# Optimization experiments

Hardware: AMD Instinct MI355X
Metric: run time of the kernel (lower is better)

The kernel has to match this reference:

```python
import jax, jax.numpy as jnp
import numpy as np

BS, C, T, H, W = 1, 64, 4, 24, 24
CH = C // 2  # half channels = 32


def setup_inputs() -> dict:
    key = jax.random.key(0)
    ks = jax.random.split(key, 6)
    s = 0.05  # small init scale keeps softmax logits well-conditioned
    return {
        "x": jax.random.normal(ks[0], (BS, C, T, H, W), dtype=jnp.float32),
        "theta_w": jax.random.normal(ks[1], (CH, C), dtype=jnp.float32) * s,
        "theta_b": jnp.zeros((CH,), dtype=jnp.float32),
        "phi_w": jax.random.normal(ks[2], (CH, C), dtype=jnp.float32) * s,
        "phi_b": jnp.zeros((CH,), dtype=jnp.float32),
        "g_w": jax.random.normal(ks[3], (CH, C), dtype=jnp.float32) * s,
        "g_b": jnp.zeros((CH,), dtype=jnp.float32),
        "k_w": jax.random.normal(ks[4], (C, CH), dtype=jnp.float32) * s,
        "k_b": jnp.zeros((C,), dtype=jnp.float32),
    }


def reference(x, theta_w, theta_b, phi_w, phi_b, g_w, g_b, k_w, k_b):
    bs, c_in, t, h, w = x.shape
    n = t * h * w
    xr = x.reshape(bs, c_in, n)  # 1x1x1 conv3d == per-position channel matmul
    v1 = jnp.einsum('oc,bcn->bon', theta_w, xr) + theta_b[:, None]  # (bs, C/2, N)
    v2 = jnp.einsum('oc,bcn->bon', phi_w, xr) + phi_b[:, None]      # (bs, C/2, N)
    gv = jnp.einsum('oc,bcn->bon', g_w, xr) + g_b[:, None]          # (bs, C/2, N)
    # per-channel rank-1 scores: score[b,c,i,j] = v1[b,c,i] * v2[b,c,j]
    scores = v1[:, :, :, None] * v2[:, :, None, :]                   # (bs, C/2, N, N)
    weights = jax.nn.softmax(scores, axis=-1)
    y = jnp.einsum('bcnm,bcm->bcn', weights, gv)                     # (bs, C/2, N)
    z = jnp.einsum('oc,bcn->bon', k_w, y) + k_b[:, None]             # (bs, C, N)
    return x + z.reshape(bs, c_in, t, h, w)
```

## Files before the change

### kernel.cpp

```cpp
#include <hip/hip_runtime.h>

#define N      2304
#define CIN    64
#define CHALF  32
#define KT     17
#define TILE   32
#define NBLK   (N / TILE)
#define NCOEF  (2 * KT * CHALF)
#define WPAD   36

__device__ __constant__ float INVF_C[KT] = {
    1.0f, 1.0f, 0.5f, 1.6666667e-1f, 4.1666668e-2f, 8.3333333e-3f,
    1.3888889e-3f, 1.9841270e-4f, 2.4801587e-5f, 2.7557319e-6f,
    2.7557319e-7f, 2.5052108e-8f, 2.0876756e-9f, 1.6059044e-10f,
    1.1470746e-11f, 7.6471637e-13f, 4.7794773e-14f };

__global__ __launch_bounds__(256) void k_momA(
    const float* __restrict__ x,
    const float* __restrict__ pw, const float* __restrict__ pb,
    const float* __restrict__ gw, const float* __restrict__ gb,
    float* __restrict__ partial)
{
    __shared__ float xs[CIN][TILE];
    __shared__ float wt2[2][CIN][WPAD];
    __shared__ float bs2[2][CHALF];
    __shared__ float bl[CHALF][33];
    __shared__ float gl[CHALF][33];

    const int tid = threadIdx.x;
    const int blk = blockIdx.x;
    const int n0  = blk * TILE;

    for (int idx = tid; idx < CIN * TILE; idx += 256) {
        int c = idx >> 5, nn = idx & 31;
        xs[c][nn] = x[c * N + n0 + nn];
    }
    for (int idx = tid; idx < 2 * CHALF * CIN; idx += 256) {
        int p = idx >> 11, rem = idx & 2047;
        int co = rem >> 6, c = rem & 63;
        wt2[p][c][co] = (p ? gw : pw)[rem];
    }
    if (tid < 2 * CHALF) {
        int p = tid >> 5, co = tid & 31;
        bs2[p][co] = (p ? gb : pb)[co];
    }
    __syncthreads();

    {
        const int pos = tid & 31;
        const int g8  = tid >> 5;
        float ab[4] = {0.f,0.f,0.f,0.f}, ag[4] = {0.f,0.f,0.f,0.f};
        #pragma unroll 4
        for (int c = 0; c < CIN; ++c) {
            float  xv = xs[c][pos];
            float4 wb = *(const float4*)&wt2[0][c][g8 * 4];
            float4 wg = *(const float4*)&wt2[1][c][g8 * 4];
            ab[0] = fmaf(wb.x, xv, ab[0]); ab[1] = fmaf(wb.y, xv, ab[1]);
            ab[2] = fmaf(wb.z, xv, ab[2]); ab[3] = fmaf(wb.w, xv, ab[3]);
            ag[0] = fmaf(wg.x, xv, ag[0]); ag[1] = fmaf(wg.y, xv, ag[1]);
            ag[2] = fmaf(wg.z, xv, ag[2]); ag[3] = fmaf(wg.w, xv, ag[3]);
        }
        #pragma unroll
        for (int k = 0; k < 4; ++k) {
            int co = g8 * 4 + k;
            bl[co][pos] = ab[k] + bs2[0][co];
            gl[co][pos] = ag[k] + bs2[1][co];
        }
    }
    __syncthreads();

    {
        const int c  = tid & 31;
        const int kg = tid >> 5;
        const int k1 = kg + 1, k2 = kg + 9;
        float d1 = 0.f, n1 = 0.f, d2 = 0.f, n2 = 0.f, n0s = 0.f;
        #pragma unroll 8
        for (int pos = 0; pos < TILE; ++pos) {
            float b  = bl[c][pos];
            float g  = gl[c][pos];
            float b2 = b * b, b4 = b2 * b2, b8 = b4 * b4;
            float p1 = (k1 & 1) ? b : 1.0f;
            p1 = (k1 & 2) ? p1 * b2 : p1;
            p1 = (k1 & 4) ? p1 * b4 : p1;
            p1 = (k1 & 8) ? p1 * b8 : p1;
            float p2 = p1 * b8;
            d1 += p1; n1 = fmaf(p1, g, n1);
            d2 += p2; n2 = fmaf(p2, g, n2);
            n0s += g;
        }
        float* pp = partial + blk * NCOEF;
        pp[k1 * 32 + c]       = d1;
        pp[544 + k1 * 32 + c] = n1;
        pp[k2 * 32 + c]       = d2;
        pp[544 + k2 * 32 + c] = n2;
        if (kg == 0) {
            pp[c]       = (float)TILE;
            pp[544 + c] = n0s;
        }
    }
}

__global__ __launch_bounds__(256) void k_evalB(
    const float* __restrict__ x,
    const float* __restrict__ tw, const float* __restrict__ tb,
    const float* __restrict__ kw, const float* __restrict__ kb,
    const float* __restrict__ partial,
    float* __restrict__ out)
{
    __shared__ float xs[CIN][TILE];
    __shared__ float wtt[CIN][WPAD];
    __shared__ float kws[CIN * CHALF];
    __shared__ float tbs[CHALF];
    __shared__ float cfl[NCOEF];
    __shared__ float al[CHALF][40];
    __shared__ float ys[CHALF][33];

    const int tid = threadIdx.x;
    const int n0  = blockIdx.x * TILE;

    for (int idx = tid; idx < CIN * TILE; idx += 256) {
        int c = idx >> 5, nn = idx & 31;
        xs[c][nn] = x[c * N + n0 + nn];
    }
    for (int idx = tid; idx < CHALF * CIN; idx += 256) {
        int co = idx >> 6, c = idx & 63;
        wtt[c][co] = tw[idx];
    }
    for (int idx = tid; idx < CIN * CHALF; idx += 256)
        kws[idx] = kw[idx];
    if (tid < CHALF) tbs[tid] = tb[tid];

    for (int t = tid; t < NCOEF / 4; t += 256) {
        float4 v = make_float4(0.f, 0.f, 0.f, 0.f);
        for (int s = 0; s < NBLK; ++s) {
            float4 p = *(const float4*)&partial[s * NCOEF + t * 4];
            v.x += p.x; v.y += p.y; v.z += p.z; v.w += p.w;
        }
        int idx = t * 4;
        int k = (idx < 544) ? (idx >> 5) : ((idx - 544) >> 5);
        float f = INVF_C[k];
        v.x *= f; v.y *= f; v.z *= f; v.w *= f;
        *(float4*)&cfl[idx] = v;
    }
    __syncthreads();

    {
        const int pos = tid & 31;
        const int g8  = tid >> 5;
        float aa[4] = {0.f,0.f,0.f,0.f};
        #pragma unroll 4
        for (int c = 0; c < CIN; ++c) {
            float  xv = xs[c][pos];
            float4 wv = *(const float4*)&wtt[c][g8 * 4];
            aa[0] = fmaf(wv.x, xv, aa[0]); aa[1] = fmaf(wv.y, xv, aa[1]);
            aa[2] = fmaf(wv.z, xv, aa[2]); aa[3] = fmaf(wv.w, xv, aa[3]);
        }
        #pragma unroll
        for (int k = 0; k < 4; ++k) {
            int co = g8 * 4 + k;
            al[co][pos] = aa[k] + tbs[co];
        }
    }
    __syncthreads();

    {
        const int c = tid >> 3;
        const int l = tid & 7;
        float dc[KT], nc[KT];
        #pragma unroll
        for (int k = 0; k < KT; ++k) {
            dc[k] = cfl[k * 32 + c];
            nc[k] = cfl[544 + k * 32 + c];
        }
        #pragma unroll
        for (int p = 0; p < 4; ++p) {
            int   ii = l + 8 * p;
            float a  = al[c][ii];
            float den = dc[KT - 1], num = nc[KT - 1];
            #pragma unroll
            for (int k = KT - 2; k >= 0; --k) {
                den = fmaf(den, a, dc[k]);
                num = fmaf(num, a, nc[k]);
            }
            ys[c][ii] = num / den;
        }
    }
    __syncthreads();

    {
        const int ii = tid & 31;
        const int cg = tid >> 5;
        float yv[CHALF];
        #pragma unroll
        for (int c = 0; c < CHALF; ++c) yv[c] = ys[c][ii];

        #pragma unroll
        for (int p = 0; p < 8; ++p) {
            int   co = cg * 8 + p;
            float z  = kb[co];
            const float4* kr = (const float4*)&kws[co * CHALF];
            #pragma unroll
            for (int c4 = 0; c4 < CHALF / 4; ++c4) {
                float4 kv = kr[c4];
                z = fmaf(kv.x, yv[c4 * 4 + 0], z);
                z = fmaf(kv.y, yv[c4 * 4 + 1], z);
                z = fmaf(kv.z, yv[c4 * 4 + 2], z);
                z = fmaf(kv.w, yv[c4 * 4 + 3], z);
            }
            out[co * N + n0 + ii] = xs[co][ii] + z;
        }
    }
}

extern "C" void kernel_launch(void* const* d_in, const int* in_sizes, int n_in,
                              void* d_out, int out_size, void* d_ws, size_t ws_size,
                              hipStream_t stream)
{
    const float* x  = (const float*)d_in[0];
    const float* tw = (const float*)d_in[1];
    const float* tb = (const float*)d_in[2];
    const float* pw = (const float*)d_in[3];
    const float* pb = (const float*)d_in[4];
    const float* gw = (const float*)d_in[5];
    const float* gb = (const float*)d_in[6];
    const float* kw = (const float*)d_in[7];
    const float* kb = (const float*)d_in[8];
    float* out = (float*)d_out;

    float* partial = (float*)d_ws;

    k_momA<<<dim3(NBLK), dim3(256), 0, stream>>>(
        x, pw, pb, gw, gb, partial);

    k_evalB<<<dim3(NBLK), dim3(256), 0, stream>>>(
        x, tw, tb, kw, kb, partial, out);
}
```

Baseline: 24.18 us.

## Move theta projection into first kernel and register-tile channel matmuls

The theta projection (v1) is now computed in the moment kernel alongside phi and g and written to workspace, so the evaluation kernel no longer loads x and theta weights to recompute it. Both 1x1 channel matmuls now use 4x4 register tiles with float4 shared-memory loads in place of per-position scalar loops. The output projection splits the channel reduction across two thread halves and combines them through shared memory. This trades extra global traffic for v1 and an added barrier against less redundant staging and more arithmetic per shared-memory load.

Result: faster. 22.84 us (-5.6%).

```diff
diff --git a/kernel.cpp b/kernel.cpp
--- a/kernel.cpp
+++ b/kernel.cpp
@@ -7,7 +7,7 @@
 #define TILE   32
 #define NBLK   (N / TILE)
 #define NCOEF  (2 * KT * CHALF)
-#define WPAD   36
+#define NCOL   (NCOEF / 4)
 
 __device__ __constant__ float INVF_C[KT] = {
     1.0f, 1.0f, 0.5f, 1.6666667e-1f, 4.1666668e-2f, 8.3333333e-3f,
@@ -17,15 +17,16 @@
 
 __global__ __launch_bounds__(256) void k_momA(
     const float* __restrict__ x,
+    const float* __restrict__ tw, const float* __restrict__ tb,
     const float* __restrict__ pw, const float* __restrict__ pb,
     const float* __restrict__ gw, const float* __restrict__ gb,
-    float* __restrict__ partial)
+    float* __restrict__ v1, float* __restrict__ partial)
 {
     __shared__ float xs[CIN][TILE];
-    __shared__ float wt2[2][CIN][WPAD];
-    __shared__ float bs2[2][CHALF];
-    __shared__ float bl[CHALF][33];
-    __shared__ float gl[CHALF][33];
+    __shared__ float wt3[3][CIN][36];
+    __shared__ float bs3[3][CHALF];
+    __shared__ float bl[CHALF][36];
+    __shared__ float gl[CHALF][36];
 
     const int tid = threadIdx.x;
     const int blk = blockIdx.x;
@@ -35,36 +36,56 @@
         int c = idx >> 5, nn = idx & 31;
         xs[c][nn] = x[c * N + n0 + nn];
     }
-    for (int idx = tid; idx < 2 * CHALF * CIN; idx += 256) {
+    for (int idx = tid; idx < 3 * CHALF * CIN; idx += 256) {
         int p = idx >> 11, rem = idx & 2047;
         int co = rem >> 6, c = rem & 63;
-        wt2[p][c][co] = (p ? gw : pw)[rem];
-    }
-    if (tid < 2 * CHALF) {
+        const float* w = (p == 0) ? tw : (p == 1) ? pw : gw;
+        wt3[p][c][co] = w[rem];
+    }
+    if (tid < 3 * CHALF) {
         int p = tid >> 5, co = tid & 31;
-        bs2[p][co] = (p ? gb : pb)[co];
-    }
-    __syncthreads();
-
-    {
-        const int pos = tid & 31;
-        const int g8  = tid >> 5;
-        float ab[4] = {0.f,0.f,0.f,0.f}, ag[4] = {0.f,0.f,0.f,0.f};
+        const float* b = (p == 0) ? tb : (p == 1) ? pb : gb;
+        bs3[p][co] = b[co];
+    }
+    __syncthreads();
+
+    if (tid < 192) {
+        const int pog = tid & 7;
+        const int cog = (tid >> 3) & 7;
+        const int pj  = tid >> 6;
+
+        float acc[4][4];
+        #pragma unroll
+        for (int i = 0; i < 4; ++i)
+            #pragma unroll
+            for (int j = 0; j < 4; ++j) acc[i][j] = 0.f;
+
         #pragma unroll 4
         for (int c = 0; c < CIN; ++c) {
-            float  xv = xs[c][pos];
-            float4 wb = *(const float4*)&wt2[0][c][g8 * 4];
-            float4 wg = *(const float4*)&wt2[1][c][g8 * 4];
-            ab[0] = fmaf(wb.x, xv, ab[0]); ab[1] = fmaf(wb.y, xv, ab[1]);
-            ab[2] = fmaf(wb.z, xv, ab[2]); ab[3] = fmaf(wb.w, xv, ab[3]);
-            ag[0] = fmaf(wg.x, xv, ag[0]); ag[1] = fmaf(wg.y, xv, ag[1]);
-            ag[2] = fmaf(wg.z, xv, ag[2]); ag[3] = fmaf(wg.w, xv, ag[3]);
-        }
-        #pragma unroll
-        for (int k = 0; k < 4; ++k) {
-            int co = g8 * 4 + k;
-            bl[co][pos] = ab[k] + bs2[0][co];
-            gl[co][pos] = ag[k] + bs2[1][co];
+            float4 xv = *(const float4*)&xs[c][pog * 4];
+            float4 wv = *(const float4*)&wt3[pj][c][cog * 4];
+            acc[0][0]=fmaf(wv.x,xv.x,acc[0][0]); acc[0][1]=fmaf(wv.x,xv.y,acc[0][1]);
+            acc[0][2]=fmaf(wv.x,xv.z,acc[0][2]); acc[0][3]=fmaf(wv.x,xv.w,acc[0][3]);
+            acc[1][0]=fmaf(wv.y,xv.x,acc[1][0]); acc[1][1]=fmaf(wv.y,xv.y,acc[1][1]);
+            acc[1][2]=fmaf(wv.y,xv.z,acc[1][2]); acc[1][3]=fmaf(wv.y,xv.w,acc[1][3]);
+            acc[2][0]=fmaf(wv.z,xv.x,acc[2][0]); acc[2][1]=fmaf(wv.z,xv.y,acc[2][1]);
+            acc[2][2]=fmaf(wv.z,xv.z,acc[2][2]); acc[2][3]=fmaf(wv.z,xv.w,acc[2][3]);
+            acc[3][0]=fmaf(wv.w,xv.x,acc[3][0]); acc[3][1]=fmaf(wv.w,xv.y,acc[3][1]);
+            acc[3][2]=fmaf(wv.w,xv.z,acc[3][2]); acc[3][3]=fmaf(wv.w,xv.w,acc[3][3]);
+        }
+        #pragma unroll
+        for (int i = 0; i < 4; ++i) {
+            int   co = cog * 4 + i;
+            float bb = bs3[pj][co];
+            float4 r = make_float4(acc[i][0] + bb, acc[i][1] + bb,
+                                   acc[i][2] + bb, acc[i][3] + bb);
+            if (pj == 0) {
+                *(float4*)&v1[co * N + n0 + pog * 4] = r;
+            } else if (pj == 1) {
+                *(float4*)&bl[co][pog * 4] = r;
+            } else {
+                *(float4*)&gl[co][pog * 4] = r;
+            }
         }
     }
     __syncthreads();
@@ -72,27 +93,32 @@
     {
         const int c  = tid & 31;
         const int kg = tid >> 5;
-        const int k1 = kg + 1, k2 = kg + 9;
+        const int k1 = kg + 1;
         float d1 = 0.f, n1 = 0.f, d2 = 0.f, n2 = 0.f, n0s = 0.f;
-        #pragma unroll 8
-        for (int pos = 0; pos < TILE; ++pos) {
-            float b  = bl[c][pos];
-            float g  = gl[c][pos];
-            float b2 = b * b, b4 = b2 * b2, b8 = b4 * b4;
-            float p1 = (k1 & 1) ? b : 1.0f;
-            p1 = (k1 & 2) ? p1 * b2 : p1;
-            p1 = (k1 & 4) ? p1 * b4 : p1;
-            p1 = (k1 & 8) ? p1 * b8 : p1;
-            float p2 = p1 * b8;
-            d1 += p1; n1 = fmaf(p1, g, n1);
-            d2 += p2; n2 = fmaf(p2, g, n2);
-            n0s += g;
+        #pragma unroll
+        for (int pq = 0; pq < 8; ++pq) {
+            float4 b4 = *(const float4*)&bl[c][pq * 4];
+            float4 g4 = *(const float4*)&gl[c][pq * 4];
+            #pragma unroll
+            for (int e = 0; e < 4; ++e) {
+                float b = (e == 0) ? b4.x : (e == 1) ? b4.y : (e == 2) ? b4.z : b4.w;
+                float g = (e == 0) ? g4.x : (e == 1) ? g4.y : (e == 2) ? g4.z : g4.w;
+                float b2 = b * b, b4v = b2 * b2, b8 = b4v * b4v;
+                float p1 = (k1 & 1) ? b : 1.0f;
+                p1 = (k1 & 2) ? p1 * b2  : p1;
+                p1 = (k1 & 4) ? p1 * b4v : p1;
+                p1 = (k1 & 8) ? p1 * b8  : p1;
+                float p2 = p1 * b8;
+                d1 += p1; n1 = fmaf(p1, g, n1);
+                d2 += p2; n2 = fmaf(p2, g, n2);
+                n0s += g;
+            }
         }
         float* pp = partial + blk * NCOEF;
-        pp[k1 * 32 + c]       = d1;
-        pp[544 + k1 * 32 + c] = n1;
-        pp[k2 * 32 + c]       = d2;
-        pp[544 + k2 * 32 + c] = n2;
+        pp[k1 * 32 + c]             = d1;
+        pp[544 + k1 * 32 + c]       = n1;
+        pp[(k1 + 8) * 32 + c]       = d2;
+        pp[544 + (k1 + 8) * 32 + c] = n2;
         if (kg == 0) {
             pp[c]       = (float)TILE;
             pp[544 + c] = n0s;
@@ -102,41 +128,32 @@
 
 __global__ __launch_bounds__(256) void k_evalB(
     const float* __restrict__ x,
-    const float* __restrict__ tw, const float* __restrict__ tb,
     const float* __restrict__ kw, const float* __restrict__ kb,
-    const float* __restrict__ partial,
+    const float* __restrict__ v1, const float* __restrict__ partial,
     float* __restrict__ out)
 {
-    __shared__ float xs[CIN][TILE];
-    __shared__ float wtt[CIN][WPAD];
-    __shared__ float kws[CIN * CHALF];
-    __shared__ float tbs[CHALF];
+    __shared__ float kwt[CHALF][68];
     __shared__ float cfl[NCOEF];
-    __shared__ float al[CHALF][40];
-    __shared__ float ys[CHALF][33];
+    __shared__ float ys[CHALF][36];
+    __shared__ float kbs[CIN];
+    __shared__ float zred[8][16][16];
 
     const int tid = threadIdx.x;
     const int n0  = blockIdx.x * TILE;
 
-    for (int idx = tid; idx < CIN * TILE; idx += 256) {
-        int c = idx >> 5, nn = idx & 31;
-        xs[c][nn] = x[c * N + n0 + nn];
-    }
-    for (int idx = tid; idx < CHALF * CIN; idx += 256) {
-        int co = idx >> 6, c = idx & 63;
-        wtt[c][co] = tw[idx];
-    }
-    for (int idx = tid; idx < CIN * CHALF; idx += 256)
-        kws[idx] = kw[idx];
-    if (tid < CHALF) tbs[tid] = tb[tid];
-
-    for (int t = tid; t < NCOEF / 4; t += 256) {
+    for (int idx = tid; idx < CIN * CHALF; idx += 256) {
+        int co = idx >> 5, c = idx & 31;
+        kwt[c][co] = kw[idx];
+    }
+    if (tid < CIN) kbs[tid] = kb[tid];
+
+    for (int col = tid; col < NCOL; col += 256) {
         float4 v = make_float4(0.f, 0.f, 0.f, 0.f);
         for (int s = 0; s < NBLK; ++s) {
-            float4 p = *(const float4*)&partial[s * NCOEF + t * 4];
+            float4 p = *(const float4*)&partial[s * NCOEF + col * 4];
             v.x += p.x; v.y += p.y; v.z += p.z; v.w += p.w;
         }
-        int idx = t * 4;
+        int idx = col * 4;
         int k = (idx < 544) ? (idx >> 5) : ((idx - 544) >> 5);
         float f = INVF_C[k];
         v.x *= f; v.y *= f; v.z *= f; v.w *= f;
@@ -145,69 +162,79 @@
     __syncthreads();
 
     {
-        const int pos = tid & 31;
-        const int g8  = tid >> 5;
-        float aa[4] = {0.f,0.f,0.f,0.f};
-        #pragma unroll 4
-        for (int c = 0; c < CIN; ++c) {
-            float  xv = xs[c][pos];
-            float4 wv = *(const float4*)&wtt[c][g8 * 4];
-            aa[0] = fmaf(wv.x, xv, aa[0]); aa[1] = fmaf(wv.y, xv, aa[1]);
-            aa[2] = fmaf(wv.z, xv, aa[2]); aa[3] = fmaf(wv.w, xv, aa[3]);
-        }
-        #pragma unroll
-        for (int k = 0; k < 4; ++k) {
-            int co = g8 * 4 + k;
-            al[co][pos] = aa[k] + tbs[co];
-        }
-    }
-    __syncthreads();
-
-    {
-        const int c = tid >> 3;
-        const int l = tid & 7;
+        const int c  = tid >> 3;
+        const int pq = tid & 7;
         float dc[KT], nc[KT];
         #pragma unroll
         for (int k = 0; k < KT; ++k) {
             dc[k] = cfl[k * 32 + c];
             nc[k] = cfl[544 + k * 32 + c];
         }
-        #pragma unroll
-        for (int p = 0; p < 4; ++p) {
-            int   ii = l + 8 * p;
-            float a  = al[c][ii];
+        float4 a4 = *(const float4*)&v1[c * N + n0 + pq * 4];
+        float4 r;
+        #pragma unroll
+        for (int e = 0; e < 4; ++e) {
+            float a = (e == 0) ? a4.x : (e == 1) ? a4.y : (e == 2) ? a4.z : a4.w;
             float den = dc[KT - 1], num = nc[KT - 1];
             #pragma unroll
             for (int k = KT - 2; k >= 0; --k) {
                 den = fmaf(den, a, dc[k]);
                 num = fmaf(num, a, nc[k]);
             }
-            ys[c][ii] = num / den;
-        }
+            float yv = num / den;
+            if (e == 0) r.x = yv; else if (e == 1) r.y = yv;
+            else if (e == 2) r.z = yv; else r.w = yv;
+        }
+        *(float4*)&ys[c][pq * 4] = r;
     }
     __syncthreads();
 
     {
-        const int ii = tid & 31;
-        const int cg = tid >> 5;
-        float yv[CHALF];
-        #pragma unroll
-        for (int c = 0; c < CHALF; ++c) yv[c] = ys[c][ii];
-
-        #pragma unroll
-        for (int p = 0; p < 8; ++p) {
-            int   co = cg * 8 + p;
-            float z  = kb[co];
-            const float4* kr = (const float4*)&kws[co * CHALF];
-            #pragma unroll
-            for (int c4 = 0; c4 < CHALF / 4; ++c4) {
-                float4 kv = kr[c4];
-                z = fmaf(kv.x, yv[c4 * 4 + 0], z);
-                z = fmaf(kv.y, yv[c4 * 4 + 1], z);
-                z = fmaf(kv.z, yv[c4 * 4 + 2], z);
-                z = fmaf(kv.w, yv[c4 * 4 + 3], z);
-            }
-            out[co * N + n0 + ii] = xs[co][ii] + z;
+        const int posq = tid & 7;
+        const int coq  = (tid >> 3) & 15;
+        const int ch   = tid >> 7;
+        float acc[4][4];
+        #pragma unroll
+        for (int i = 0; i < 4; ++i)
+            #pragma unroll
+            for (int j = 0; j < 4; ++j) acc[i][j] = 0.f;
+
+        #pragma unroll 4
+        for (int i = 0; i < 16; ++i) {
+            int c = ch * 16 + i;
+            float4 yv = *(const float4*)&ys[c][posq * 4];
+            float4 wv = *(const float4*)&kwt[c][coq * 4];
+            acc[0][0]=fmaf(wv.x,yv.x,acc[0][0]); acc[0][1]=fmaf(wv.x,yv.y,acc[0][1]);
+            acc[0][2]=fmaf(wv.x,yv.z,acc[0][2]); acc[0][3]=fmaf(wv.x,yv.w,acc[0][3]);
+            acc[1][0]=fmaf(wv.y,yv.x,acc[1][0]); acc[1][1]=fmaf(wv.y,yv.y,acc[1][1]);
+            acc[1][2]=fmaf(wv.y,yv.z,acc[1][2]); acc[1][3]=fmaf(wv.y,yv.w,acc[1][3]);
+            acc[2][0]=fmaf(wv.z,yv.x,acc[2][0]); acc[2][1]=fmaf(wv.z,yv.y,acc[2][1]);
+            acc[2][2]=fmaf(wv.z,yv.z,acc[2][2]); acc[2][3]=fmaf(wv.z,yv.w,acc[2][3]);
+            acc[3][0]=fmaf(wv.w,yv.x,acc[3][0]); acc[3][1]=fmaf(wv.w,yv.y,acc[3][1]);
+            acc[3][2]=fmaf(wv.w,yv.z,acc[3][2]); acc[3][3]=fmaf(wv.w,yv.w,acc[3][3]);
+        }
+
+        if (ch == 1) {
+            #pragma unroll
+            for (int i = 0; i < 4; ++i)
+                *(float4*)&zred[posq][coq][i * 4] =
+                    make_float4(acc[i][0], acc[i][1], acc[i][2], acc[i][3]);
+        }
+        __syncthreads();
+        if (ch == 0) {
+            #pragma unroll
+            for (int i = 0; i < 4; ++i) {
+                int    co  = coq * 4 + i;
+                float  kbv = kbs[co];
+                float4 zo  = *(const float4*)&zred[posq][coq][i * 4];
+                float4 xv  = *(const float4*)&x[co * N + n0 + posq * 4];
+                float4 o;
+                o.x = xv.x + acc[i][0] + zo.x + kbv;
+                o.y = xv.y + acc[i][1] + zo.y + kbv;
+                o.z = xv.z + acc[i][2] + zo.z + kbv;
+                o.w = xv.w + acc[i][3] + zo.w + kbv;
+                *(float4*)&out[co * N + n0 + posq * 4] = o;
+            }
         }
     }
 }
@@ -227,11 +254,13 @@
     const float* kb = (const float*)d_in[8];
     float* out = (float*)d_out;
 
-    float* partial = (float*)d_ws;
+    float* ws      = (float*)d_ws;
+    float* v1      = ws;
+    float* partial = ws + 73728;
 
     k_momA<<<dim3(NBLK), dim3(256), 0, stream>>>(
-        x, pw, pb, gw, gb, partial);
+        x, tw, tb, pw, pb, gw, gb, v1, partial);
 
     k_evalB<<<dim3(NBLK), dim3(256), 0, stream>>>(
-        x, tw, tb, kw, kb, partial, out);
+        x, kw, kb, v1, partial, out);
 }
```
